# Kernel tuning notes

Measured on AMD Instinct MI355X. Metric: run time of the kernel, lower is better.

The kernel has to match this reference:

```python
import jax, jax.numpy as jnp
import numpy as np

TOP_K = 4
N_ROUTED = 32          # routed experts
ZERO_EXPERTS = 8       # identity zero experts
HIDDEN = 2048
INTER = 1024
TOKENS = 1024
RSF = 1.0              # routed_scaling_factor


def setup_inputs() -> dict:
    key = jax.random.key(0)
    ks = jax.random.split(key, 6)
    s = 0.02
    e_tot = N_ROUTED + ZERO_EXPERTS
    return {
        "hidden_states": jax.random.normal(ks[0], (TOKENS, HIDDEN), jnp.float32),
        "router_w": jax.random.normal(ks[1], (e_tot, HIDDEN), jnp.float32) * s,
        "correction_bias": jax.random.normal(ks[2], (e_tot,), jnp.float32) * s,
        "w1_gate": jax.random.normal(ks[3], (N_ROUTED, INTER, HIDDEN), jnp.float32) * s,
        "w1_up": jax.random.normal(ks[4], (N_ROUTED, INTER, HIDDEN), jnp.float32) * s,
        "w2": jax.random.normal(ks[5], (N_ROUTED, HIDDEN, INTER), jnp.float32) * s,
    }


def reference(hidden_states, router_w, correction_bias, w1_gate, w1_up, w2):
    e_routed = w1_gate.shape[0]
    # Router (fp32): logits -> sigmoid scores; select top-k on scores + correction bias,
    # routing weights are the raw sigmoid scores (renormalize=False).
    logits = hidden_states.astype(jnp.float32) @ router_w.T          # [T, E_tot]
    scores = jax.nn.sigmoid(logits)
    _, topk_ids = jax.lax.top_k(scores + correction_bias[None, :], TOP_K)
    topk_w = jnp.take_along_axis(scores, topk_ids, axis=1)           # [T, K]
    # Combine matrix [T, E_tot]: per-token weight for each expert (0 if not selected).
    onehot = jax.nn.one_hot(topk_ids, scores.shape[1], dtype=hidden_states.dtype)
    combine = jnp.sum(onehot * topk_w[..., None].astype(hidden_states.dtype), axis=1)
    # Routed experts: SwiGLU FFN per expert, weighted combine.
    g = jnp.einsum('th,eih->eti', hidden_states, w1_gate)            # [E, T, I]
    u = jnp.einsum('th,eih->eti', hidden_states, w1_up)
    h = jax.nn.silu(g) * u
    ye = jnp.einsum('eti,ehi->eth', h, w2)                           # [E, T, H]
    routed = jnp.einsum('eth,te->th', ye, combine[:, :e_routed])
    # Zero experts (identity): weight * hidden_states.
    zero = hidden_states * jnp.sum(combine[:, e_routed:], axis=1, keepdims=True)
    return (routed + zero) * RSF
```

## Files before the change

kernel.cpp:

```cpp
#include <hip/hip_runtime.h>
#include <hip/hip_bf16.h>
#include <cstdint>

#define T_TOK 1024
#define HID   2048
#define INTER 1024
#define NEXP  32
#define NTOT  40
#define RSF   1.0f

typedef short bf16x8 __attribute__((ext_vector_type(8)));
typedef float f32x4  __attribute__((ext_vector_type(4)));

__device__ inline short f2bf(float f) {
    unsigned x = __builtin_bit_cast(unsigned, f);
    x += 0x7fffu + ((x >> 16) & 1u);
    return (short)(x >> 16);
}

__global__ __launch_bounds__(256) void k_router(
    const float* __restrict__ hs, const float* __restrict__ rw,
    const float* __restrict__ cb, int* __restrict__ topk_ids,
    float* __restrict__ topk_w, float* __restrict__ zero_w,
    int* __restrict__ counts)
{
    int t = blockIdx.x;
    __shared__ float hrow[HID];
    __shared__ float sc[NTOT];
    const float* h = hs + (size_t)t * HID;
    for (int i = threadIdx.x; i < HID / 4; i += 256)
        ((float4*)hrow)[i] = ((const float4*)h)[i];
    __syncthreads();
    int wid = threadIdx.x >> 6, lane = threadIdx.x & 63;
    for (int e = wid; e < NTOT; e += 4) {
        const float* w = rw + (size_t)e * HID;
        float p = 0.f;
        for (int k = lane; k < HID; k += 64) p += hrow[k] * w[k];
        for (int s = 32; s; s >>= 1) p += __shfl_down(p, s, 64);
        if (lane == 0) sc[e] = 1.f / (1.f + expf(-p));
    }
    __syncthreads();
    if (threadIdx.x == 0) {
        float key[NTOT];
        for (int e = 0; e < NTOT; e++) key[e] = sc[e] + cb[e];
        float zw = 0.f;
        for (int k = 0; k < 4; k++) {
            int best = 0; float bv = key[0];
            for (int e = 1; e < NTOT; e++)
                if (key[e] > bv) { bv = key[e]; best = e; }
            key[best] = -1e30f;
            topk_ids[t * 4 + k] = best;
            float wv = sc[best];
            topk_w[t * 4 + k] = wv;
            if (best >= NEXP) zw += wv;
            else atomicAdd(&counts[best], 1);
        }
        zero_w[t] = zw * RSF;
    }
}

__global__ void k_prefix(const int* __restrict__ counts, int* __restrict__ offsets)
{
    if (threadIdx.x == 0 && blockIdx.x == 0) {
        int acc = 0;
        for (int e = 0; e < NEXP; e++) {
            offsets[e] = acc;
            acc += (counts[e] + 127) & ~127;
        }
        offsets[NEXP] = acc;
    }
}

__global__ void k_scatter(const int* __restrict__ topk_ids, const float* __restrict__ topk_w,
                          const int* __restrict__ offsets, int* __restrict__ cnt2,
                          int* __restrict__ btok, float* __restrict__ bw)
{
    int t = blockIdx.x * 256 + threadIdx.x;
    if (t >= T_TOK) return;
    for (int k = 0; k < 4; k++) {
        int e = topk_ids[t * 4 + k];
        if (e < NEXP) {
            int pos  = atomicAdd(&cnt2[e], 1);
            int slot = offsets[e] + pos;
            btok[slot] = t;
            bw[slot]   = topk_w[t * 4 + k];
        }
    }
}

__global__ __launch_bounds__(256, 2) void k_ffn1(
    const float* __restrict__ hs, const float* __restrict__ w1g, const float* __restrict__ w1u,
    const int* __restrict__ counts, const int* __restrict__ offsets,
    const int* __restrict__ btok, unsigned short* __restrict__ Hbuf)
{
    int e = blockIdx.z, mt = blockIdx.y, it = blockIdx.x;
    int ne = counts[e];
    if (mt * 128 >= ne) return;
    int base  = offsets[e] + mt * 128;
    int valid = ne - mt * 128; if (valid > 128) valid = 128;

    __shared__ __align__(16) char smem[65536];
    short* At  = (short*)smem;
    short* Bt  = (short*)(smem + 8192);
    int*   tok = (int*)(smem + 16384);
    float* Cb  = (float*)smem;

    int tid = threadIdx.x;
    if (tid < 128) tok[tid] = (tid < valid) ? btok[base + tid] : btok[base];
    __syncthreads();

    const float* wg = w1g + (size_t)e * INTER * HID + (size_t)(it * 64) * HID;
    const float* wu = w1u + (size_t)e * INTER * HID + (size_t)(it * 64) * HID;

    const float* aptr[4]; short* adst[4];
    const float* bptr[4]; short* bdst[4];
#pragma unroll
    for (int u = 0; u < 4; u++) {
        int idx = tid + u * 256;
        int r = idx >> 3, seg = idx & 7;
        aptr[u] = hs + (size_t)tok[r] * HID + seg * 4;
        adst[u] = At + r * 32 + seg * 4;
        bptr[u] = (r < 64 ? wg + (size_t)r * HID : wu + (size_t)(r - 64) * HID) + seg * 4;
        bdst[u] = Bt + r * 32 + seg * 4;
    }

    int wid = tid >> 6, lane = tid & 63;
    int wrow = (wid >> 1) * 64, wcol = (wid & 1) * 64;
    int lrow = lane & 15, quad = lane >> 4;
    f32x4 acc[4][4];
#pragma unroll
    for (int mi = 0; mi < 4; mi++)
#pragma unroll
        for (int ni = 0; ni < 4; ni++) acc[mi][ni] = 0.f;

    for (int k0 = 0; k0 < HID; k0 += 32) {
#pragma unroll
        for (int u = 0; u < 4; u++) {
            float4 va = *(const float4*)(aptr[u] + k0);
            float4 vb = *(const float4*)(bptr[u] + k0);
            *(short4*)adst[u] = make_short4(f2bf(va.x), f2bf(va.y), f2bf(va.z), f2bf(va.w));
            *(short4*)bdst[u] = make_short4(f2bf(vb.x), f2bf(vb.y), f2bf(vb.z), f2bf(vb.w));
        }
        __syncthreads();
        bf16x8 af[4], bfr[4];
#pragma unroll
        for (int mi = 0; mi < 4; mi++)
            af[mi] = *(bf16x8*)(At + (wrow + mi * 16 + lrow) * 32 + quad * 8);
#pragma unroll
        for (int ni = 0; ni < 4; ni++)
            bfr[ni] = *(bf16x8*)(Bt + (wcol + ni * 16 + lrow) * 32 + quad * 8);
#pragma unroll
        for (int mi = 0; mi < 4; mi++)
#pragma unroll
            for (int ni = 0; ni < 4; ni++)
                acc[mi][ni] = __builtin_amdgcn_mfma_f32_16x16x32_bf16(af[mi], bfr[ni], acc[mi][ni], 0, 0, 0);
        __syncthreads();
    }

#pragma unroll
    for (int mi = 0; mi < 4; mi++)
#pragma unroll
        for (int ni = 0; ni < 4; ni++)
#pragma unroll
            for (int r = 0; r < 4; r++)
                Cb[(wrow + mi * 16 + quad * 4 + r) * 128 + (wcol + ni * 16 + lrow)] = acc[mi][ni][r];
    __syncthreads();
    for (int idx = tid; idx < 128 * 64; idx += 256) {
        int m = idx >> 6, c = idx & 63;
        float g = Cb[m * 128 + c];
        float u = Cb[m * 128 + 64 + c];
        float h = g / (1.f + __expf(-g)) * u;
        Hbuf[(size_t)(base + m) * INTER + it * 64 + c] = (unsigned short)f2bf(h);
    }
}

__global__ void k_init_out(const float* __restrict__ hs, const float* __restrict__ zw,
                           float* __restrict__ out)
{
    int idx = blockIdx.x * 256 + threadIdx.x;
    int t = idx >> 9;
    float4 v = ((const float4*)hs)[idx];
    float s = zw[t];
    v.x *= s; v.y *= s; v.z *= s; v.w *= s;
    ((float4*)out)[idx] = v;
}

__global__ __launch_bounds__(256, 2) void k_ffn2(
    const unsigned short* __restrict__ Hbuf, const float* __restrict__ w2,
    const int* __restrict__ counts, const int* __restrict__ offsets,
    const int* __restrict__ btok, const float* __restrict__ bw,
    float* __restrict__ out)
{
    int e = blockIdx.z, mt = blockIdx.y, ht = blockIdx.x;
    int ne = counts[e];
    if (mt * 128 >= ne) return;
    int base  = offsets[e] + mt * 128;
    int valid = ne - mt * 128; if (valid > 128) valid = 128;

    __shared__ __align__(16) short At[128 * 32];
    __shared__ __align__(16) short Bt[128 * 32];
    __shared__ int   tok[128];
    __shared__ float wgt[128];

    int tid = threadIdx.x;
    if (tid < 128) {
        tok[tid] = (tid < valid) ? btok[base + tid] : btok[base];
        wgt[tid] = (tid < valid) ? bw[base + tid] : 0.f;
    }
    __syncthreads();

    const float* w2e = w2 + (size_t)e * HID * INTER;
    const unsigned short* asrc[2]; short* adst[2];
#pragma unroll
    for (int u = 0; u < 2; u++) {
        int idx = tid + u * 256;
        int r = idx >> 2, seg = idx & 3;
        asrc[u] = Hbuf + (size_t)(base + r) * INTER + seg * 8;
        adst[u] = At + r * 32 + seg * 8;
    }
    const float* bptr[4]; short* bdst[4];
#pragma unroll
    for (int u = 0; u < 4; u++) {
        int idx = tid + u * 256;
        int r = idx >> 3, seg = idx & 7;
        bptr[u] = w2e + (size_t)(ht * 128 + r) * INTER + seg * 4;
        bdst[u] = Bt + r * 32 + seg * 4;
    }

    int wid = tid >> 6, lane = tid & 63;
    int wrow = (wid >> 1) * 64, wcol = (wid & 1) * 64;
    int lrow = lane & 15, quad = lane >> 4;
    f32x4 acc[4][4];
#pragma unroll
    for (int mi = 0; mi < 4; mi++)
#pragma unroll
        for (int ni = 0; ni < 4; ni++) acc[mi][ni] = 0.f;

    for (int k0 = 0; k0 < INTER; k0 += 32) {
#pragma unroll
        for (int u = 0; u < 2; u++) {
            int4 v = *(const int4*)(asrc[u] + k0);
            *(int4*)adst[u] = v;
        }
#pragma unroll
        for (int u = 0; u < 4; u++) {
            float4 vb = *(const float4*)(bptr[u] + k0);
            *(short4*)bdst[u] = make_short4(f2bf(vb.x), f2bf(vb.y), f2bf(vb.z), f2bf(vb.w));
        }
        __syncthreads();
        bf16x8 af[4], bfr[4];
#pragma unroll
        for (int mi = 0; mi < 4; mi++)
            af[mi] = *(bf16x8*)(At + (wrow + mi * 16 + lrow) * 32 + quad * 8);
#pragma unroll
        for (int ni = 0; ni < 4; ni++)
            bfr[ni] = *(bf16x8*)(Bt + (wcol + ni * 16 + lrow) * 32 + quad * 8);
#pragma unroll
        for (int mi = 0; mi < 4; mi++)
#pragma unroll
            for (int ni = 0; ni < 4; ni++)
                acc[mi][ni] = __builtin_amdgcn_mfma_f32_16x16x32_bf16(af[mi], bfr[ni], acc[mi][ni], 0, 0, 0);
        __syncthreads();
    }

#pragma unroll
    for (int mi = 0; mi < 4; mi++) {
#pragma unroll
        for (int r = 0; r < 4; r++) {
            int m = wrow + mi * 16 + quad * 4 + r;
            if (m < valid) {
                int   t = tok[m];
                float w = wgt[m] * RSF;
#pragma unroll
                for (int ni = 0; ni < 4; ni++) {
                    int col = ht * 128 + wcol + ni * 16 + lrow;
                    atomicAdd(&out[(size_t)t * HID + col], acc[mi][ni][r] * w);
                }
            }
        }
    }
}

extern "C" void kernel_launch(void* const* d_in, const int* in_sizes, int n_in,
                              void* d_out, int out_size, void* d_ws, size_t ws_size,
                              hipStream_t stream)
{
    const float* hs  = (const float*)d_in[0];
    const float* rw  = (const float*)d_in[1];
    const float* cb  = (const float*)d_in[2];
    const float* w1g = (const float*)d_in[3];
    const float* w1u = (const float*)d_in[4];
    const float* w2  = (const float*)d_in[5];
    float* out = (float*)d_out;

    char* ws = (char*)d_ws;
    int*   counts   = (int*)(ws + 0);
    int*   cnt2     = (int*)(ws + 128);
    int*   offsets  = (int*)(ws + 256);
    int*   topk_ids = (int*)(ws + 4096);
    float* topk_w   = (float*)(ws + 20480);
    float* zero_w   = (float*)(ws + 36864);
    int*   btok     = (int*)(ws + 40960);
    float* bww      = (float*)(ws + 73728);
    unsigned short* Hbuf = (unsigned short*)(ws + 131072);

    hipMemsetAsync(d_ws, 0, 4096, stream);

    k_router<<<T_TOK, 256, 0, stream>>>(hs, rw, cb, topk_ids, topk_w, zero_w, counts);
    k_prefix<<<1, 64, 0, stream>>>(counts, offsets);
    k_scatter<<<4, 256, 0, stream>>>(topk_ids, topk_w, offsets, cnt2, btok, bww);
    k_ffn1<<<dim3(16, 8, 32), 256, 0, stream>>>(hs, w1g, w1u, counts, offsets, btok, Hbuf);
    k_init_out<<<(T_TOK * HID / 4) / 256, 256, 0, stream>>>(hs, zero_w, out);
    k_ffn2<<<dim3(16, 8, 32), 256, 0, stream>>>(Hbuf, w2, counts, offsets, btok, bww, out);
}
```

Measured before the change: 953.0 us.

## Double-buffer and swizzle MoE GEMM tiles, pre-convert hidden states to bf16

Adds a kernel that converts hidden states to bf16 once, so ffn1 gathers bf16 rows instead of converting fp32 in every tile. Both expert GEMMs now use double-buffered, XOR-swizzled LDS tiles with register prefetch of the next K slice, and occupancy is raised to 4 blocks per SM. ffn1 interleaves gate and up rows so the SwiGLU epilogue runs in registers via a lane shuffle instead of staging through shared memory. Expert segments are no longer padded to 128, and the grid order changes to (tile, expert, m-tile). The router loop is vectorised with float4 loads.

```diff
diff --git a/kernel.cpp b/kernel.cpp
--- a/kernel.cpp
+++ b/kernel.cpp
@@ -1,5 +1,4 @@
 #include <hip/hip_runtime.h>
-#include <hip/hip_bf16.h>
 #include <cstdint>
 
 #define T_TOK 1024
@@ -18,6 +17,20 @@
     return (short)(x >> 16);
 }
 
+__global__ __launch_bounds__(256) void k_cvt_hs(const float* __restrict__ hs,
+                                                unsigned short* __restrict__ hsb)
+{
+    int idx = blockIdx.x * 256 + threadIdx.x;
+    const float4* s = (const float4*)hs + (size_t)idx * 2;
+    float4 a = s[0], b = s[1];
+    union { unsigned short u[8]; int4 v; } r;
+    r.u[0] = (unsigned short)f2bf(a.x); r.u[1] = (unsigned short)f2bf(a.y);
+    r.u[2] = (unsigned short)f2bf(a.z); r.u[3] = (unsigned short)f2bf(a.w);
+    r.u[4] = (unsigned short)f2bf(b.x); r.u[5] = (unsigned short)f2bf(b.y);
+    r.u[6] = (unsigned short)f2bf(b.z); r.u[7] = (unsigned short)f2bf(b.w);
+    ((int4*)hsb)[idx] = r.v;
+}
+
 __global__ __launch_bounds__(256) void k_router(
     const float* __restrict__ hs, const float* __restrict__ rw,
     const float* __restrict__ cb, int* __restrict__ topk_ids,
@@ -25,17 +38,19 @@
     int* __restrict__ counts)
 {
     int t = blockIdx.x;
-    __shared__ float hrow[HID];
+    __shared__ float4 hrow[HID / 4];
     __shared__ float sc[NTOT];
-    const float* h = hs + (size_t)t * HID;
-    for (int i = threadIdx.x; i < HID / 4; i += 256)
-        ((float4*)hrow)[i] = ((const float4*)h)[i];
+    const float4* h4 = (const float4*)(hs + (size_t)t * HID);
+    for (int i = threadIdx.x; i < HID / 4; i += 256) hrow[i] = h4[i];
     __syncthreads();
     int wid = threadIdx.x >> 6, lane = threadIdx.x & 63;
     for (int e = wid; e < NTOT; e += 4) {
-        const float* w = rw + (size_t)e * HID;
+        const float4* w4 = (const float4*)(rw + (size_t)e * HID);
         float p = 0.f;
-        for (int k = lane; k < HID; k += 64) p += hrow[k] * w[k];
+        for (int c = lane; c < HID / 4; c += 64) {
+            float4 a = w4[c], b = hrow[c];
+            p += a.x * b.x + a.y * b.y + a.z * b.z + a.w * b.w;
+        }
         for (int s = 32; s; s >>= 1) p += __shfl_down(p, s, 64);
         if (lane == 0) sc[e] = 1.f / (1.f + expf(-p));
     }
@@ -63,10 +78,7 @@
 {
     if (threadIdx.x == 0 && blockIdx.x == 0) {
         int acc = 0;
-        for (int e = 0; e < NEXP; e++) {
-            offsets[e] = acc;
-            acc += (counts[e] + 127) & ~127;
-        }
+        for (int e = 0; e < NEXP; e++) { offsets[e] = acc; acc += counts[e]; }
         offsets[NEXP] = acc;
     }
 }
@@ -88,89 +100,130 @@
     }
 }
 
-__global__ __launch_bounds__(256, 2) void k_ffn1(
-    const float* __restrict__ hs, const float* __restrict__ w1g, const float* __restrict__ w1u,
-    const int* __restrict__ counts, const int* __restrict__ offsets,
-    const int* __restrict__ btok, unsigned short* __restrict__ Hbuf)
-{
-    int e = blockIdx.z, mt = blockIdx.y, it = blockIdx.x;
+#define SWZ(row, seg) (((row) * 32) + (((seg) ^ ((row) & 3)) * 8))
+
+__global__ __launch_bounds__(256, 4) void k_ffn1(
+    const unsigned short* __restrict__ hsb, const float* __restrict__ w1g,
+    const float* __restrict__ w1u, const int* __restrict__ counts,
+    const int* __restrict__ offsets, const int* __restrict__ btok,
+    unsigned short* __restrict__ Hbuf)
+{
+    int it = blockIdx.x, e = blockIdx.y, mt = blockIdx.z;
     int ne = counts[e];
     if (mt * 128 >= ne) return;
     int base  = offsets[e] + mt * 128;
     int valid = ne - mt * 128; if (valid > 128) valid = 128;
 
-    __shared__ __align__(16) char smem[65536];
-    short* At  = (short*)smem;
-    short* Bt  = (short*)(smem + 8192);
-    int*   tok = (int*)(smem + 16384);
-    float* Cb  = (float*)smem;
+    __shared__ __align__(16) short At[2][128 * 32];
+    __shared__ __align__(16) short Bt[2][128 * 32];
+    __shared__ int tok[128];
 
     int tid = threadIdx.x;
     if (tid < 128) tok[tid] = (tid < valid) ? btok[base + tid] : btok[base];
     __syncthreads();
 
-    const float* wg = w1g + (size_t)e * INTER * HID + (size_t)(it * 64) * HID;
-    const float* wu = w1u + (size_t)e * INTER * HID + (size_t)(it * 64) * HID;
-
-    const float* aptr[4]; short* adst[4];
-    const float* bptr[4]; short* bdst[4];
-#pragma unroll
-    for (int u = 0; u < 4; u++) {
+    const unsigned short* asrc[2]; int adst[2];
+#pragma unroll
+    for (int u = 0; u < 2; u++) {
         int idx = tid + u * 256;
-        int r = idx >> 3, seg = idx & 7;
-        aptr[u] = hs + (size_t)tok[r] * HID + seg * 4;
-        adst[u] = At + r * 32 + seg * 4;
-        bptr[u] = (r < 64 ? wg + (size_t)r * HID : wu + (size_t)(r - 64) * HID) + seg * 4;
-        bdst[u] = Bt + r * 32 + seg * 4;
-    }
+        int r = idx >> 2, s = idx & 3;
+        asrc[u] = hsb + (size_t)tok[r] * HID + s * 8;
+        adst[u] = SWZ(r, s);
+    }
+
+    int br_ = tid >> 1, half = tid & 1;
+    const float* bsrc = ((br_ & 1) ? w1u : w1g)
+                      + (size_t)e * INTER * HID
+                      + (size_t)(it * 64 + (br_ >> 1)) * HID + half * 16;
+    int bdst0 = SWZ(br_, half * 2);
+    int bdst1 = SWZ(br_, half * 2 + 1);
+
+    f32x4 acc[4][4];
+#pragma unroll
+    for (int mi = 0; mi < 4; mi++)
+#pragma unroll
+        for (int ni = 0; ni < 4; ni++) acc[mi][ni] = 0.f;
 
     int wid = tid >> 6, lane = tid & 63;
     int wrow = (wid >> 1) * 64, wcol = (wid & 1) * 64;
     int lrow = lane & 15, quad = lane >> 4;
-    f32x4 acc[4][4];
-#pragma unroll
-    for (int mi = 0; mi < 4; mi++)
-#pragma unroll
-        for (int ni = 0; ni < 4; ni++) acc[mi][ni] = 0.f;
-
-    for (int k0 = 0; k0 < HID; k0 += 32) {
-#pragma unroll
-        for (int u = 0; u < 4; u++) {
-            float4 va = *(const float4*)(aptr[u] + k0);
-            float4 vb = *(const float4*)(bptr[u] + k0);
-            *(short4*)adst[u] = make_short4(f2bf(va.x), f2bf(va.y), f2bf(va.z), f2bf(va.w));
-            *(short4*)bdst[u] = make_short4(f2bf(vb.x), f2bf(vb.y), f2bf(vb.z), f2bf(vb.w));
+
+    int4  an[2];
+    float4 bn[4];
+#pragma unroll
+    for (int u = 0; u < 2; u++) an[u] = *(const int4*)asrc[u];
+#pragma unroll
+    for (int u = 0; u < 4; u++) bn[u] = *(const float4*)(bsrc + u * 4);
+#pragma unroll
+    for (int u = 0; u < 2; u++) *(int4*)&At[0][adst[u]] = an[u];
+    {
+        union { short s[8]; int4 v; } p0, p1;
+        p0.s[0]=f2bf(bn[0].x); p0.s[1]=f2bf(bn[0].y); p0.s[2]=f2bf(bn[0].z); p0.s[3]=f2bf(bn[0].w);
+        p0.s[4]=f2bf(bn[1].x); p0.s[5]=f2bf(bn[1].y); p0.s[6]=f2bf(bn[1].z); p0.s[7]=f2bf(bn[1].w);
+        p1.s[0]=f2bf(bn[2].x); p1.s[1]=f2bf(bn[2].y); p1.s[2]=f2bf(bn[2].z); p1.s[3]=f2bf(bn[2].w);
+        p1.s[4]=f2bf(bn[3].x); p1.s[5]=f2bf(bn[3].y); p1.s[6]=f2bf(bn[3].z); p1.s[7]=f2bf(bn[3].w);
+        *(int4*)&Bt[0][bdst0] = p0.v;
+        *(int4*)&Bt[0][bdst1] = p1.v;
+    }
+    __syncthreads();
+
+    int cur = 0;
+    for (int kt = 0; kt < HID / 32; kt++) {
+        bool pf = (kt < HID / 32 - 1);
+        if (pf) {
+            int k0n = (kt + 1) * 32;
+#pragma unroll
+            for (int u = 0; u < 2; u++) an[u] = *(const int4*)(asrc[u] + k0n);
+#pragma unroll
+            for (int u = 0; u < 4; u++) bn[u] = *(const float4*)(bsrc + k0n + u * 4);
+        }
+        bf16x8 bfr[4];
+#pragma unroll
+        for (int ni = 0; ni < 4; ni++) {
+            int rb = wcol + ni * 16 + lrow;
+            bfr[ni] = *(bf16x8*)&Bt[cur][SWZ(rb, quad)];
+        }
+#pragma unroll
+        for (int mi = 0; mi < 4; mi++) {
+            int ra = wrow + mi * 16 + lrow;
+            bf16x8 af = *(bf16x8*)&At[cur][SWZ(ra, quad)];
+#pragma unroll
+            for (int ni = 0; ni < 4; ni++)
+                acc[mi][ni] = __builtin_amdgcn_mfma_f32_16x16x32_bf16(af, bfr[ni], acc[mi][ni], 0, 0, 0);
+        }
+        if (pf) {
+#pragma unroll
+            for (int u = 0; u < 2; u++) *(int4*)&At[cur ^ 1][adst[u]] = an[u];
+            union { short s[8]; int4 v; } p0, p1;
+            p0.s[0]=f2bf(bn[0].x); p0.s[1]=f2bf(bn[0].y); p0.s[2]=f2bf(bn[0].z); p0.s[3]=f2bf(bn[0].w);
+            p0.s[4]=f2bf(bn[1].x); p0.s[5]=f2bf(bn[1].y); p0.s[6]=f2bf(bn[1].z); p0.s[7]=f2bf(bn[1].w);
+            p1.s[0]=f2bf(bn[2].x); p1.s[1]=f2bf(bn[2].y); p1.s[2]=f2bf(bn[2].z); p1.s[3]=f2bf(bn[2].w);
+            p1.s[4]=f2bf(bn[3].x); p1.s[5]=f2bf(bn[3].y); p1.s[6]=f2bf(bn[3].z); p1.s[7]=f2bf(bn[3].w);
+            *(int4*)&Bt[cur ^ 1][bdst0] = p0.v;
+            *(int4*)&Bt[cur ^ 1][bdst1] = p1.v;
         }
         __syncthreads();
-        bf16x8 af[4], bfr[4];
-#pragma unroll
-        for (int mi = 0; mi < 4; mi++)
-            af[mi] = *(bf16x8*)(At + (wrow + mi * 16 + lrow) * 32 + quad * 8);
-#pragma unroll
-        for (int ni = 0; ni < 4; ni++)
-            bfr[ni] = *(bf16x8*)(Bt + (wcol + ni * 16 + lrow) * 32 + quad * 8);
-#pragma unroll
-        for (int mi = 0; mi < 4; mi++)
-#pragma unroll
-            for (int ni = 0; ni < 4; ni++)
-                acc[mi][ni] = __builtin_amdgcn_mfma_f32_16x16x32_bf16(af[mi], bfr[ni], acc[mi][ni], 0, 0, 0);
-        __syncthreads();
-    }
-
-#pragma unroll
-    for (int mi = 0; mi < 4; mi++)
-#pragma unroll
-        for (int ni = 0; ni < 4; ni++)
-#pragma unroll
-            for (int r = 0; r < 4; r++)
-                Cb[(wrow + mi * 16 + quad * 4 + r) * 128 + (wcol + ni * 16 + lrow)] = acc[mi][ni][r];
-    __syncthreads();
-    for (int idx = tid; idx < 128 * 64; idx += 256) {
-        int m = idx >> 6, c = idx & 63;
-        float g = Cb[m * 128 + c];
-        float u = Cb[m * 128 + 64 + c];
-        float h = g / (1.f + __expf(-g)) * u;
-        Hbuf[(size_t)(base + m) * INTER + it * 64 + c] = (unsigned short)f2bf(h);
+        cur ^= 1;
+    }
+
+#pragma unroll
+    for (int mi = 0; mi < 4; mi++) {
+#pragma unroll
+        for (int ni = 0; ni < 4; ni++) {
+#pragma unroll
+            for (int rr = 0; rr < 4; rr++) {
+                float v = acc[mi][ni][rr];
+                float o = __shfl_xor(v, 1, 64);
+                int m = wrow + mi * 16 + quad * 4 + rr;
+                if (!(lrow & 1) && m < valid) {
+                    float g = v;
+                    float h = g / (1.f + __expf(-g)) * o;
+                    int col = wcol + ni * 16 + lrow;
+                    Hbuf[(size_t)(base + m) * INTER + it * 64 + (col >> 1)] =
+                        (unsigned short)f2bf(h);
+                }
+            }
+        }
     }
 }
 
@@ -185,97 +238,125 @@
     ((float4*)out)[idx] = v;
 }
 
-__global__ __launch_bounds__(256, 2) void k_ffn2(
+__global__ __launch_bounds__(256, 4) void k_ffn2(
     const unsigned short* __restrict__ Hbuf, const float* __restrict__ w2,
     const int* __restrict__ counts, const int* __restrict__ offsets,
     const int* __restrict__ btok, const float* __restrict__ bw,
     float* __restrict__ out)
 {
-    int e = blockIdx.z, mt = blockIdx.y, ht = blockIdx.x;
+    int ht = blockIdx.x, e = blockIdx.y, mt = blockIdx.z;
     int ne = counts[e];
     if (mt * 128 >= ne) return;
     int base  = offsets[e] + mt * 128;
     int valid = ne - mt * 128; if (valid > 128) valid = 128;
 
-    __shared__ __align__(16) short At[128 * 32];
-    __shared__ __align__(16) short Bt[128 * 32];
+    __shared__ __align__(16) short At[2][128 * 32];
+    __shared__ __align__(16) short Bt[2][128 * 32];
     __shared__ int   tok[128];
     __shared__ float wgt[128];
 
     int tid = threadIdx.x;
     if (tid < 128) {
-        tok[tid] = (tid < valid) ? btok[base + tid] : btok[base];
-        wgt[tid] = (tid < valid) ? bw[base + tid] : 0.f;
-    }
-    __syncthreads();
-
-    const float* w2e = w2 + (size_t)e * HID * INTER;
-    const unsigned short* asrc[2]; short* adst[2];
+        tok[tid] = (tid < valid) ? btok[base + tid] : 0;
+        wgt[tid] = (tid < valid) ? bw[base + tid] * RSF : 0.f;
+    }
+    __syncthreads();
+
+    const unsigned short* asrc[2]; int adst[2];
 #pragma unroll
     for (int u = 0; u < 2; u++) {
         int idx = tid + u * 256;
-        int r = idx >> 2, seg = idx & 3;
-        asrc[u] = Hbuf + (size_t)(base + r) * INTER + seg * 8;
-        adst[u] = At + r * 32 + seg * 8;
-    }
-    const float* bptr[4]; short* bdst[4];
-#pragma unroll
-    for (int u = 0; u < 4; u++) {
-        int idx = tid + u * 256;
-        int r = idx >> 3, seg = idx & 7;
-        bptr[u] = w2e + (size_t)(ht * 128 + r) * INTER + seg * 4;
-        bdst[u] = Bt + r * 32 + seg * 4;
-    }
+        int r = idx >> 2, s = idx & 3;
+        asrc[u] = Hbuf + (size_t)(base + r) * INTER + s * 8;
+        adst[u] = SWZ(r, s);
+    }
+
+    int br_ = tid >> 1, half = tid & 1;
+    const float* bsrc = w2 + (size_t)e * HID * INTER
+                      + (size_t)(ht * 128 + br_) * INTER + half * 16;
+    int bdst0 = SWZ(br_, half * 2);
+    int bdst1 = SWZ(br_, half * 2 + 1);
+
+    f32x4 acc[4][4];
+#pragma unroll
+    for (int mi = 0; mi < 4; mi++)
+#pragma unroll
+        for (int ni = 0; ni < 4; ni++) acc[mi][ni] = 0.f;
 
     int wid = tid >> 6, lane = tid & 63;
     int wrow = (wid >> 1) * 64, wcol = (wid & 1) * 64;
     int lrow = lane & 15, quad = lane >> 4;
-    f32x4 acc[4][4];
-#pragma unroll
-    for (int mi = 0; mi < 4; mi++)
-#pragma unroll
-        for (int ni = 0; ni < 4; ni++) acc[mi][ni] = 0.f;
-
-    for (int k0 = 0; k0 < INTER; k0 += 32) {
-#pragma unroll
-        for (int u = 0; u < 2; u++) {
-            int4 v = *(const int4*)(asrc[u] + k0);
-            *(int4*)adst[u] = v;
-        }
-#pragma unroll
-        for (int u = 0; u < 4; u++) {
-            float4 vb = *(const float4*)(bptr[u] + k0);
-            *(short4*)bdst[u] = make_short4(f2bf(vb.x), f2bf(vb.y), f2bf(vb.z), f2bf(vb.w));
+
+    int4  an[2];
+    float4 bn[4];
+#pragma unroll
+    for (int u = 0; u < 2; u++) an[u] = *(const int4*)asrc[u];
+#pragma unroll
+    for (int u = 0; u < 4; u++) bn[u] = *(const float4*)(bsrc + u * 4);
+#pragma unroll
+    for (int u = 0; u < 2; u++) *(int4*)&At[0][adst[u]] = an[u];
+    {
+        union { short s[8]; int4 v; } p0, p1;
+        p0.s[0]=f2bf(bn[0].x); p0.s[1]=f2bf(bn[0].y); p0.s[2]=f2bf(bn[0].z); p0.s[3]=f2bf(bn[0].w);
+        p0.s[4]=f2bf(bn[1].x); p0.s[5]=f2bf(bn[1].y); p0.s[6]=f2bf(bn[1].z); p0.s[7]=f2bf(bn[1].w);
+        p1.s[0]=f2bf(bn[2].x); p1.s[1]=f2bf(bn[2].y); p1.s[2]=f2bf(bn[2].z); p1.s[3]=f2bf(bn[2].w);
+        p1.s[4]=f2bf(bn[3].x); p1.s[5]=f2bf(bn[3].y); p1.s[6]=f2bf(bn[3].z); p1.s[7]=f2bf(bn[3].w);
+        *(int4*)&Bt[0][bdst0] = p0.v;
+        *(int4*)&Bt[0][bdst1] = p1.v;
+    }
+    __syncthreads();
+
+    int cur = 0;
+    for (int kt = 0; kt < INTER / 32; kt++) {
+        bool pf = (kt < INTER / 32 - 1);
+        if (pf) {
+            int k0n = (kt + 1) * 32;
+#pragma unroll
+            for (int u = 0; u < 2; u++) an[u] = *(const int4*)(asrc[u] + k0n);
+#pragma unroll
+            for (int u = 0; u < 4; u++) bn[u] = *(const float4*)(bsrc + k0n + u * 4);
+        }
+        bf16x8 bfr[4];
+#pragma unroll
+        for (int ni = 0; ni < 4; ni++) {
+            int rb = wcol + ni * 16 + lrow;
+            bfr[ni] = *(bf16x8*)&Bt[cur][SWZ(rb, quad)];
+        }
+#pragma unroll
+        for (int mi = 0; mi < 4; mi++) {
+            int ra = wrow + mi * 16 + lrow;
+            bf16x8 af = *(bf16x8*)&At[cur][SWZ(ra, quad)];
+#pragma unroll
+            for (int ni = 0; ni < 4; ni++)
+                acc[mi][ni] = __builtin_amdgcn_mfma_f32_16x16x32_bf16(af, bfr[ni], acc[mi][ni], 0, 0, 0);
+        }
+        if (pf) {
+#pragma unroll
+            for (int u = 0; u < 2; u++) *(int4*)&At[cur ^ 1][adst[u]] = an[u];
+            union { short s[8]; int4 v; } p0, p1;
+            p0.s[0]=f2bf(bn[0].x); p0.s[1]=f2bf(bn[0].y); p0.s[2]=f2bf(bn[0].z); p0.s[3]=f2bf(bn[0].w);
+            p0.s[4]=f2bf(bn[1].x); p0.s[5]=f2bf(bn[1].y); p0.s[6]=f2bf(bn[1].z); p0.s[7]=f2bf(bn[1].w);
+            p1.s[0]=f2bf(bn[2].x); p1.s[1]=f2bf(bn[2].y); p1.s[2]=f2bf(bn[2].z); p1.s[3]=f2bf(bn[2].w);
+            p1.s[4]=f2bf(bn[3].x); p1.s[5]=f2bf(bn[3].y); p1.s[6]=f2bf(bn[3].z); p1.s[7]=f2bf(bn[3].w);
+            *(int4*)&Bt[cur ^ 1][bdst0] = p0.v;
+            *(int4*)&Bt[cur ^ 1][bdst1] = p1.v;
         }
         __syncthreads();
-        bf16x8 af[4], bfr[4];
-#pragma unroll
-        for (int mi = 0; mi < 4; mi++)
-            af[mi] = *(bf16x8*)(At + (wrow + mi * 16 + lrow) * 32 + quad * 8);
-#pragma unroll
-        for (int ni = 0; ni < 4; ni++)
-            bfr[ni] = *(bf16x8*)(Bt + (wcol + ni * 16 + lrow) * 32 + quad * 8);
-#pragma unroll
-        for (int mi = 0; mi < 4; mi++)
-#pragma unroll
-            for (int ni = 0; ni < 4; ni++)
-                acc[mi][ni] = __builtin_amdgcn_mfma_f32_16x16x32_bf16(af[mi], bfr[ni], acc[mi][ni], 0, 0, 0);
-        __syncthreads();
+        cur ^= 1;
     }
 
 #pragma unroll
     for (int mi = 0; mi < 4; mi++) {
 #pragma unroll
-        for (int r = 0; r < 4; r++) {
-            int m = wrow + mi * 16 + quad * 4 + r;
+        for (int rr = 0; rr < 4; rr++) {
+            int m = wrow + mi * 16 + quad * 4 + rr;
             if (m < valid) {
                 int   t = tok[m];
-                float w = wgt[m] * RSF;
-#pragma unroll
-                for (int ni = 0; ni < 4; ni++) {
-                    int col = ht * 128 + wcol + ni * 16 + lrow;
-                    atomicAdd(&out[(size_t)t * HID + col], acc[mi][ni][r] * w);
-                }
+                float w = wgt[m];
+                float* orow = out + (size_t)t * HID + ht * 128;
+#pragma unroll
+                for (int ni = 0; ni < 4; ni++)
+                    atomicAdd(&orow[wcol + ni * 16 + lrow], acc[mi][ni][rr] * w);
             }
         }
     }
@@ -302,14 +383,16 @@
     float* zero_w   = (float*)(ws + 36864);
     int*   btok     = (int*)(ws + 40960);
     float* bww      = (float*)(ws + 73728);
-    unsigned short* Hbuf = (unsigned short*)(ws + 131072);
+    unsigned short* hsb  = (unsigned short*)(ws + 131072);
+    unsigned short* Hbuf = (unsigned short*)(ws + 131072 + (size_t)T_TOK * HID * 2);
 
     hipMemsetAsync(d_ws, 0, 4096, stream);
 
+    k_cvt_hs<<<T_TOK * HID / 8 / 256, 256, 0, stream>>>(hs, hsb);
     k_router<<<T_TOK, 256, 0, stream>>>(hs, rw, cb, topk_ids, topk_w, zero_w, counts);
     k_prefix<<<1, 64, 0, stream>>>(counts, offsets);
     k_scatter<<<4, 256, 0, stream>>>(topk_ids, topk_w, offsets, cnt2, btok, bww);
-    k_ffn1<<<dim3(16, 8, 32), 256, 0, stream>>>(hs, w1g, w1u, counts, offsets, btok, Hbuf);
+    k_ffn1<<<dim3(16, 32, 8), 256, 0, stream>>>(hsb, w1g, w1u, counts, offsets, btok, Hbuf);
     k_init_out<<<(T_TOK * HID / 4) / 256, 256, 0, stream>>>(hs, zero_w, out);
-    k_ffn2<<<dim3(16, 8, 32), 256, 0, stream>>>(Hbuf, w2, counts, offsets, btok, bww, out);
-}
+    k_ffn2<<<dim3(16, 32, 8), 256, 0, stream>>>(Hbuf, w2, counts, offsets, btok, bww, out);
+}
```

Result: faster. 824.1 us (-13.5%).
